# Kernel tuning notes

Measured on AMD Instinct MI355X. Metric: run time of the kernel, lower is better.

The kernel has to match this reference:

```python
import jax, jax.numpy as jnp
import numpy as np

N, E, G, H = 50000, 800000, 64, 4
IN_DIM, HID, OUT = 768, 256, 128
EPS = 1e-5
SLOPE = 0.2


def _glorot(k, shape):
    lim = np.sqrt(6.0 / (shape[0] + shape[1])).astype(np.float32)
    return jax.random.uniform(k, shape, jnp.float32, -lim, lim)


def setup_inputs() -> dict:
    key = jax.random.key(0)
    ks = jax.random.split(key, 24)
    inp = {
        'x': jax.random.normal(ks[0], (N, IN_DIM), jnp.float32),
        'edge_index': jax.random.randint(ks[1], (2, E), 0, N, jnp.int32),
        'batch': jnp.sort(jax.random.randint(ks[2], (N,), 0, G, jnp.int32)),
    }
    dims = [(IN_DIM, HID), (HID, HID), (HID, OUT)]
    for i, (di, do) in enumerate(dims, start=1):
        c = do // H
        inp[f'W{i}'] = _glorot(ks[3 * i], (di, do))
        inp[f'asrc{i}'] = _glorot(ks[3 * i + 1], (H, c))
        inp[f'adst{i}'] = _glorot(ks[3 * i + 2], (H, c))
        inp[f'b{i}'] = jnp.zeros((do,), jnp.float32)
        inp[f'g{i}'] = jnp.ones((do,), jnp.float32)
        inp[f'be{i}'] = jnp.zeros((do,), jnp.float32)
    return inp


def gat_conv(x, src, dst, W, asrc, adst, b):
    # PyG GATConv, concat=True, negative_slope=0.2, self-loops pre-appended.
    n = x.shape[0]
    HC = W.shape[1]
    C = HC // H
    h = (x @ W).reshape(n, H, C)                 # [N,H,C]
    e_src = (h * asrc).sum(-1)                   # [N,H]
    e_dst = (h * adst).sum(-1)                   # [N,H]
    e = jax.nn.leaky_relu(e_src[src] + e_dst[dst], SLOPE)  # [E',H]
    m = jax.ops.segment_max(e, dst, num_segments=n)
    p = jnp.exp(e - m[dst])
    denom = jax.ops.segment_sum(p, dst, num_segments=n)
    alpha = p / denom[dst]                       # segment softmax over in-edges
    out = jax.ops.segment_sum(alpha[:, :, None] * h[src], dst, num_segments=n)
    return out.reshape(n, HC) + b


def layer_norm(x, g, b):
    mu = x.mean(-1, keepdims=True)
    var = x.var(-1, keepdims=True)
    return g * (x - mu) * jax.lax.rsqrt(var + EPS) + b


def reference(x, edge_index, batch, W1, asrc1, adst1, b1, g1, be1,
              W2, asrc2, adst2, b2, g2, be2, W3, asrc3, adst3, b3, g3, be3):
    n = x.shape[0]
    loops = jnp.arange(n, dtype=edge_index.dtype)
    src = jnp.concatenate([edge_index[0], loops])
    dst = jnp.concatenate([edge_index[1], loops])
    h = gat_conv(x, src, dst, W1, asrc1, adst1, b1)
    h = layer_norm(jax.nn.elu(h), g1, be1)
    h = gat_conv(h, src, dst, W2, asrc2, adst2, b2)
    h = layer_norm(jax.nn.elu(h), g2, be2)
    h = gat_conv(h, src, dst, W3, asrc3, adst3, b3)
    node_emb = layer_norm(h, g3, be3)
    s = jax.ops.segment_sum(node_emb, batch, num_segments=G)
    cnt = jax.ops.segment_sum(jnp.ones((n, 1), node_emb.dtype), batch, num_segments=G)
    graph_emb = s / jnp.maximum(cnt, 1.0)
    return (node_emb, graph_emb)
```

## Files before the change

### kernel.cpp

```cpp
#include <hip/hip_runtime.h>
#include <math.h>

__device__ __forceinline__ float lrelu(float v) { return v > 0.f ? v : 0.2f * v; }
__device__ __forceinline__ float bf2f(ushort u) {
    return __uint_as_float(((unsigned int)u) << 16);
}
__device__ __forceinline__ ushort f2bf(float f) {
    unsigned int x = __float_as_uint(f);
    return (ushort)((x + 0x7fffu + ((x >> 16) & 1u)) >> 16);
}
__device__ __forceinline__ float wave_allred_sum(float v) {
#pragma unroll
    for (int off = 1; off < 64; off <<= 1) v += __shfl_xor(v, off, 64);
    return v;
}

typedef short bf16x8 __attribute__((ext_vector_type(8)));
typedef float f32x4 __attribute__((ext_vector_type(4)));

typedef const __attribute__((address_space(1))) void* gas_ptr;
typedef __attribute__((address_space(3))) void* las_ptr;
__device__ __forceinline__ void gload_lds16(const void* g, void* l) {
    __builtin_amdgcn_global_load_lds((gas_ptr)g, (las_ptr)l, 16, 0, 0);
}

__global__ void hist_kernel(const int* __restrict__ dstrow, int* __restrict__ cnt,
                            int Etot, int E) {
    int i = blockIdx.x * blockDim.x + threadIdx.x;
    if (i >= Etot) return;
    int d = (i < E) ? dstrow[i] : (i - E);
    atomicAdd(&cnt[d], 1);
}

__global__ __launch_bounds__(256) void scan1_kernel(const int* __restrict__ cnt,
                                                    int* __restrict__ out,
                                                    int* __restrict__ btot, int n) {
    __shared__ int s[256];
    int i = blockIdx.x * 256 + threadIdx.x;
    int v = (i < n) ? cnt[i] : 0;
    s[threadIdx.x] = v;
    __syncthreads();
    for (int off = 1; off < 256; off <<= 1) {
        int t = (threadIdx.x >= off) ? s[threadIdx.x - off] : 0;
        __syncthreads();
        s[threadIdx.x] += t;
        __syncthreads();
    }
    if (i < n) out[i] = s[threadIdx.x];
    if (threadIdx.x == 255) btot[blockIdx.x] = s[255];
}
__global__ __launch_bounds__(1024) void scan2_kernel(int* __restrict__ btot, int nb) {
    __shared__ int s[1024];
    int tid = threadIdx.x;
    int v = (tid < nb) ? btot[tid] : 0;
    s[tid] = v;
    __syncthreads();
    for (int off = 1; off < 1024; off <<= 1) {
        int t = (tid >= off) ? s[tid - off] : 0;
        __syncthreads();
        s[tid] += t;
        __syncthreads();
    }
    if (tid < nb) btot[tid] = s[tid] - v;
}
__global__ void scan3_kernel(const int* __restrict__ scanned, const int* __restrict__ btot,
                             int* __restrict__ rowptr, int n) {
    int i = blockIdx.x * 256 + threadIdx.x;
    if (i < n) rowptr[i + 1] = scanned[i] + btot[i >> 8];
    if (i == 0) rowptr[0] = 0;
}

__global__ void fill_kernel(const int* __restrict__ srcrow, const int* __restrict__ dstrow,
                            const int* __restrict__ rowptr, int* __restrict__ pos,
                            int* __restrict__ srcs, int Etot, int E) {
    int i = blockIdx.x * blockDim.x + threadIdx.x;
    if (i >= Etot) return;
    int d = (i < E) ? dstrow[i] : (i - E);
    int s = (i < E) ? srcrow[i] : (i - E);
    int p = atomicAdd(&pos[d], 1);
    srcs[rowptr[d] + p] = s;
}

__global__ __launch_bounds__(256) void wconv_kernel(const float* __restrict__ W,
                                                    ushort* __restrict__ Wt, int K, int N) {
    __shared__ float t[32][33];
    int k0 = blockIdx.x * 32, n0 = blockIdx.y * 32;
    int tx = threadIdx.x & 31, ty = threadIdx.x >> 5;
#pragma unroll
    for (int i = 0; i < 32; i += 8)
        t[ty + i][tx] = W[(size_t)(k0 + ty + i) * N + n0 + tx];
    __syncthreads();
#pragma unroll
    for (int i = 0; i < 32; i += 8)
        Wt[(size_t)(n0 + ty + i) * K + k0 + tx] = f2bf(t[tx][ty + i]);
}

template <typename TA>
__global__ __launch_bounds__(256) void gemm_mfma2(const TA* __restrict__ A,
                                                  const ushort* __restrict__ Wt,
                                                  ushort* __restrict__ C,
                                                  int M, int K, int N) {
    constexpr bool F32A = (sizeof(TA) == 4);
    constexpr int ASZ = F32A ? 16384 : 8192;
    __shared__ __align__(16) unsigned char smem[2 * ASZ + 16384];

    int tid = threadIdx.x;
    int wv = tid >> 6, lane = tid & 63;
    int quad = lane >> 4, mrow = lane & 15;

    int nwg = gridDim.x * gridDim.y;
    int id = blockIdx.y * gridDim.x + blockIdx.x;
    int q8 = nwg >> 3, r8 = nwg & 7;
    int xcd = id & 7, loc = id >> 3;
    int wgid = (xcd < r8 ? xcd * (q8 + 1) : r8 * (q8 + 1) + (xcd - r8) * q8) + loc;
    int n0 = (wgid % gridDim.x) * 128;
    int m0 = (wgid / gridDim.x) * 128;

    f32x4 acc[2][8] = {};

    auto stageA = [&](int kt, int buf) {
        unsigned char* lb = smem + buf * ASZ;
        if constexpr (F32A) {
#pragma unroll
            for (int q = 0; q < 4; q++) {
                int row = q * 32 + (tid >> 3);
                int gch = (tid & 7) ^ (row & 7);
                int rc = min(m0 + row, M - 1);
                gload_lds16((const float*)A + (size_t)rc * K + kt + gch * 4,
                            lb + q * 4096 + tid * 16);
            }
        } else {
#pragma unroll
            for (int q = 0; q < 2; q++) {
                int row = q * 64 + (tid >> 2);
                int gch = (tid & 3) ^ ((row & 3) ^ ((row >> 2) & 1));
                int rc = min(m0 + row, M - 1);
                gload_lds16((const ushort*)A + (size_t)rc * K + kt + gch * 8,
                            lb + q * 4096 + tid * 16);
            }
        }
    };
    auto stageB = [&](int kt, int buf) {
        unsigned char* lb = smem + 2 * ASZ + buf * 8192;
#pragma unroll
        for (int q = 0; q < 2; q++) {
            int row = q * 64 + (tid >> 2);
            int gch = (tid & 3) ^ ((row & 3) ^ ((row >> 2) & 1));
            gload_lds16(Wt + (size_t)(n0 + row) * K + kt + gch * 8,
                        lb + q * 4096 + tid * 16);
        }
    };

    int nsteps = K >> 5;
    stageA(0, 0);
    stageB(0, 0);
    __syncthreads();

    for (int s = 0; s < nsteps; s++) {
        int kt = s << 5;
        if (s + 1 < nsteps) {
            stageA(kt + 32, (s + 1) & 1);
            stageB(kt + 32, (s + 1) & 1);
        }
        const unsigned char* la = smem + (s & 1) * ASZ;
        const unsigned char* lbB = smem + 2 * ASZ + (s & 1) * 8192;

        bf16x8 afrag[2], bfrag[8];
#pragma unroll
        for (int r = 0; r < 2; r++) {
            int row = wv * 32 + r * 16 + mrow;
            if constexpr (F32A) {
                int f = row & 7;
                float4 x0 = *(const float4*)(la + row * 128 + ((quad * 2 + 0) ^ f) * 16);
                float4 x1 = *(const float4*)(la + row * 128 + ((quad * 2 + 1) ^ f) * 16);
                union { bf16x8 v; ushort u[8]; } t;
                t.u[0] = f2bf(x0.x); t.u[1] = f2bf(x0.y);
                t.u[2] = f2bf(x0.z); t.u[3] = f2bf(x0.w);
                t.u[4] = f2bf(x1.x); t.u[5] = f2bf(x1.y);
                t.u[6] = f2bf(x1.z); t.u[7] = f2bf(x1.w);
                afrag[r] = t.v;
            } else {
                int f = (row & 3) ^ ((row >> 2) & 1);
                afrag[r] = *(const bf16x8*)(la + row * 64 + (quad ^ f) * 16);
            }
        }
#pragma unroll
        for (int c = 0; c < 8; c++) {
            int row = c * 16 + mrow;
            int f = (row & 3) ^ ((row >> 2) & 1);
            bfrag[c] = *(const bf16x8*)(lbB + row * 64 + (quad ^ f) * 16);
        }
#pragma unroll
        for (int r = 0; r < 2; r++)
#pragma unroll
            for (int c = 0; c < 8; c++)
                acc[r][c] = __builtin_amdgcn_mfma_f32_16x16x32_bf16(afrag[r], bfrag[c],
                                                                    acc[r][c], 0, 0, 0);
        __syncthreads();
    }

    int col = lane & 15;
#pragma unroll
    for (int r = 0; r < 2; r++) {
#pragma unroll
        for (int c = 0; c < 8; c++) {
#pragma unroll
            for (int reg = 0; reg < 4; reg++) {
                int gm = m0 + wv * 32 + r * 16 + quad * 4 + reg;
                int gn = n0 + c * 16 + col;
                if (gm < M) C[(size_t)gm * N + gn] = f2bf(acc[r][c][reg]);
            }
        }
    }
}

template <int VPL>
__global__ __launch_bounds__(256) void attn_wave(const ushort* __restrict__ H,
                                                 const float* __restrict__ asrc,
                                                 const float* __restrict__ adst,
                                                 float* __restrict__ es, float* __restrict__ ed,
                                                 int N) {
    constexpr int HC = VPL * 64;
    int lane = threadIdx.x & 63;
    int node = (blockIdx.x * blockDim.x + threadIdx.x) >> 6;
    if (node >= N) return;
    const ushort* hp = H + (size_t)node * HC + lane * VPL;
    float esum = 0.f, dsum = 0.f;
#pragma unroll
    for (int j = 0; j < VPL; j++) {
        float h = bf2f(hp[j]);
        int ch = lane * VPL + j;
        esum += h * asrc[ch];
        dsum += h * adst[ch];
    }
#pragma unroll
    for (int off = 1; off < 16; off <<= 1) {
        esum += __shfl_xor(esum, off, 64);
        dsum += __shfl_xor(dsum, off, 64);
    }
    if ((lane & 15) == 0) {
        int hh = lane >> 4;
        es[node * 4 + hh] = esum;
        ed[node * 4 + hh] = dsum;
    }
}

template <int VPL>
__global__ __launch_bounds__(256) void agg_gather(
    const ushort* __restrict__ H, const float* __restrict__ es, const float* __restrict__ ed,
    const int* __restrict__ rowptr, const int* __restrict__ srcs,
    const float* __restrict__ bias, const float* __restrict__ gamma,
    const float* __restrict__ beta, ushort* __restrict__ XoutB, float* __restrict__ XoutF,
    int N, int applyElu) {
    constexpr int HC = VPL * 64;
    int lane = threadIdx.x & 63;
    int node = (blockIdx.x * blockDim.x + threadIdx.x) >> 6;
    if (node >= N) return;
    int base = rowptr[node];
    int deg = rowptr[node + 1] - base;
    float4 ed4 = *(const float4*)&ed[node * 4];

    float4 sm = make_float4(0.f, 0.f, 0.f, 0.f);
    for (int i = lane; i < deg; i += 64) {
        int s = srcs[base + i];
        float4 e4 = *(const float4*)&es[(size_t)s * 4];
        sm.x += __expf(lrelu(e4.x + ed4.x));
        sm.y += __expf(lrelu(e4.y + ed4.y));
        sm.z += __expf(lrelu(e4.z + ed4.z));
        sm.w += __expf(lrelu(e4.w + ed4.w));
    }
    sm.x = wave_allred_sum(sm.x); sm.y = wave_allred_sum(sm.y);
    sm.z = wave_allred_sum(sm.z); sm.w = wave_allred_sum(sm.w);

    int hh = lane >> 4;
    float rd_h = 1.f / ((hh == 0) ? sm.x : (hh == 1) ? sm.y : (hh == 2) ? sm.z : sm.w);
    float edh = (hh == 0) ? ed4.x : (hh == 1) ? ed4.y : (hh == 2) ? ed4.z : ed4.w;

    float acc[VPL];
#pragma unroll
    for (int j = 0; j < VPL; j++) acc[j] = 0.f;
    const ushort* Hl = H + lane * VPL;

    int i = 0;
    for (; i + 2 <= deg; i += 2) {
        int s0 = srcs[base + i];
        int s1 = srcs[base + i + 1];
        float e0 = es[(size_t)s0 * 4 + hh];
        float e1 = es[(size_t)s1 * 4 + hh];
        const ushort* hp0 = Hl + (size_t)s0 * HC;
        const ushort* hp1 = Hl + (size_t)s1 * HC;
        float a0 = __expf(lrelu(e0 + edh)) * rd_h;
        float a1 = __expf(lrelu(e1 + edh)) * rd_h;
        if constexpr (VPL == 4) {
            ushort4 h0 = *(const ushort4*)hp0;
            ushort4 h1 = *(const ushort4*)hp1;
            acc[0] += a0 * bf2f(h0.x) + a1 * bf2f(h1.x);
            acc[1] += a0 * bf2f(h0.y) + a1 * bf2f(h1.y);
            acc[2] += a0 * bf2f(h0.z) + a1 * bf2f(h1.z);
            acc[3] += a0 * bf2f(h0.w) + a1 * bf2f(h1.w);
        } else {
            ushort2 h0 = *(const ushort2*)hp0;
            ushort2 h1 = *(const ushort2*)hp1;
            acc[0] += a0 * bf2f(h0.x) + a1 * bf2f(h1.x);
            acc[1] += a0 * bf2f(h0.y) + a1 * bf2f(h1.y);
        }
    }
    for (; i < deg; i++) {
        int s = srcs[base + i];
        float a = __expf(lrelu(es[(size_t)s * 4 + hh] + edh)) * rd_h;
        const ushort* hp = Hl + (size_t)s * HC;
        if constexpr (VPL == 4) {
            ushort4 hv = *(const ushort4*)hp;
            acc[0] += a * bf2f(hv.x); acc[1] += a * bf2f(hv.y);
            acc[2] += a * bf2f(hv.z); acc[3] += a * bf2f(hv.w);
        } else {
            ushort2 hv = *(const ushort2*)hp;
            acc[0] += a * bf2f(hv.x); acc[1] += a * bf2f(hv.y);
        }
    }

    float v[VPL];
    float s1 = 0.f, s2 = 0.f;
#pragma unroll
    for (int j = 0; j < VPL; j++) {
        int ch = lane * VPL + j;
        float t = acc[j] + bias[ch];
        if (applyElu) t = (t > 0.f) ? t : (__expf(t) - 1.f);
        v[j] = t;
        s1 += t;
        s2 += t * t;
    }
    s1 = wave_allred_sum(s1);
    s2 = wave_allred_sum(s2);
    float mu = s1 / (float)HC;
    float var = s2 / (float)HC - mu * mu;
    float rs = rsqrtf(var + 1e-5f);
#pragma unroll
    for (int j = 0; j < VPL; j++) {
        int ch = lane * VPL + j;
        float o = gamma[ch] * (v[j] - mu) * rs + beta[ch];
        if (XoutF) XoutF[(size_t)node * HC + ch] = o;
        else XoutB[(size_t)node * HC + ch] = f2bf(o);
    }
}

__global__ __launch_bounds__(128) void gsum_kernel(const float* __restrict__ node_emb,
                                                   const int* __restrict__ batch,
                                                   float* __restrict__ gsum,
                                                   int* __restrict__ gcnt, int N) {
    int start = blockIdx.x * 256;
    if (start >= N) return;
    int end = min(start + 256, N);
    int ch = threadIdx.x;
    float acc = 0.f;
    int runlen = 0;
    int curg = batch[start];
    for (int n = start; n < end; n++) {
        int g = batch[n];
        if (g != curg) {
            atomicAdd(&gsum[curg * 128 + ch], acc);
            if (ch == 0) atomicAdd(&gcnt[curg], runlen);
            acc = 0.f; runlen = 0; curg = g;
        }
        acc += node_emb[(size_t)n * 128 + ch];
        runlen++;
    }
    atomicAdd(&gsum[curg * 128 + ch], acc);
    if (ch == 0) atomicAdd(&gcnt[curg], runlen);
}

__global__ void gfinal_kernel(const float* __restrict__ gsum, const int* __restrict__ gcnt,
                              float* __restrict__ out, int Gn) {
    int i = blockIdx.x * blockDim.x + threadIdx.x;
    if (i >= Gn * 128) return;
    int g = i >> 7;
    out[i] = gsum[i] / fmaxf((float)gcnt[g], 1.f);
}

extern "C" void kernel_launch(void* const* d_in, const int* in_sizes, int n_in, void* d_out,
                              int out_size, void* d_ws, size_t ws_size, hipStream_t stream) {
    const float* x = (const float*)d_in[0];
    const int* ei = (const int*)d_in[1];
    const int* batch = (const int*)d_in[2];
    const float* W1 = (const float*)d_in[3];
    const float* as1 = (const float*)d_in[4];
    const float* ad1 = (const float*)d_in[5];
    const float* b1 = (const float*)d_in[6];
    const float* g1 = (const float*)d_in[7];
    const float* be1 = (const float*)d_in[8];
    const float* W2 = (const float*)d_in[9];
    const float* as2 = (const float*)d_in[10];
    const float* ad2 = (const float*)d_in[11];
    const float* b2 = (const float*)d_in[12];
    const float* g2 = (const float*)d_in[13];
    const float* be2 = (const float*)d_in[14];
    const float* W3 = (const float*)d_in[15];
    const float* as3 = (const float*)d_in[16];
    const float* ad3 = (const float*)d_in[17];
    const float* b3 = (const float*)d_in[18];
    const float* g3 = (const float*)d_in[19];
    const float* be3 = (const float*)d_in[20];

    int N = in_sizes[2];
    int E = in_sizes[1] / 2;
    int Etot = E + N;

    char* w = (char*)d_ws;
    size_t off = 0;
    auto alloc = [&](size_t bytes) -> void* {
        void* p = w + off;
        off += (bytes + 255) & ~(size_t)255;
        return p;
    };
    int* cnt = (int*)alloc((size_t)N * 4);
    int* pos = (int*)alloc((size_t)N * 4);
    float* gsum = (float*)alloc(64 * 128 * 4);
    int* gcnt = (int*)alloc(64 * 4);
    size_t zbytes = off;
    int* scantmp = (int*)alloc((size_t)N * 4);
    int* btot = (int*)alloc(1024 * 4);
    int* rowptr = (int*)alloc((size_t)(N + 1) * 4);
    int* srcs = (int*)alloc((size_t)Etot * 4);
    float* es = (float*)alloc((size_t)N * 16);
    float* ed = (float*)alloc((size_t)N * 16);
    ushort* Hb = (ushort*)alloc((size_t)N * 256 * 2);
    ushort* Xb = (ushort*)alloc((size_t)N * 256 * 2);
    ushort* wt1 = (ushort*)alloc((size_t)768 * 256 * 2);
    ushort* wt2 = (ushort*)alloc((size_t)256 * 256 * 2);
    ushort* wt3 = (ushort*)alloc((size_t)256 * 128 * 2);

    hipMemsetAsync(d_ws, 0, zbytes, stream);

    const int* srcrow = ei;
    const int* dstrow = ei + E;

    wconv_kernel<<<dim3(768 / 32, 256 / 32), 256, 0, stream>>>(W1, wt1, 768, 256);
    wconv_kernel<<<dim3(256 / 32, 256 / 32), 256, 0, stream>>>(W2, wt2, 256, 256);
    wconv_kernel<<<dim3(256 / 32, 128 / 32), 256, 0, stream>>>(W3, wt3, 256, 128);

    int eb = (Etot + 255) / 256;
    int nb = (N + 255) / 256;
    hist_kernel<<<eb, 256, 0, stream>>>(dstrow, cnt, Etot, E);
    scan1_kernel<<<nb, 256, 0, stream>>>(cnt, scantmp, btot, N);
    scan2_kernel<<<1, 1024, 0, stream>>>(btot, nb);
    scan3_kernel<<<nb, 256, 0, stream>>>(scantmp, btot, rowptr, N);
    fill_kernel<<<eb, 256, 0, stream>>>(srcrow, dstrow, rowptr, pos, srcs, Etot, E);

    int mT = (N + 127) / 128;
    int nodeWaveBlocks = (N + 3) / 4;

    float* out_node = (float*)d_out;
    float* out_graph = (float*)d_out + (size_t)N * 128;

    gemm_mfma2<float><<<dim3(2, mT), 256, 0, stream>>>(x, wt1, Hb, N, 768, 256);
    attn_wave<4><<<nodeWaveBlocks, 256, 0, stream>>>(Hb, as1, ad1, es, ed, N);
    agg_gather<4><<<nodeWaveBlocks, 256, 0, stream>>>(Hb, es, ed, rowptr, srcs, b1, g1, be1,
                                                      Xb, nullptr, N, 1);
    gemm_mfma2<ushort><<<dim3(2, mT), 256, 0, stream>>>(Xb, wt2, Hb, N, 256, 256);
    attn_wave<4><<<nodeWaveBlocks, 256, 0, stream>>>(Hb, as2, ad2, es, ed, N);
    agg_gather<4><<<nodeWaveBlocks, 256, 0, stream>>>(Hb, es, ed, rowptr, srcs, b2, g2, be2,
                                                      Xb, nullptr, N, 1);
    gemm_mfma2<ushort><<<dim3(1, mT), 256, 0, stream>>>(Xb, wt3, Hb, N, 256, 128);
    attn_wave<2><<<nodeWaveBlocks, 256, 0, stream>>>(Hb, as3, ad3, es, ed, N);
    agg_gather<2><<<nodeWaveBlocks, 256, 0, stream>>>(Hb, es, ed, rowptr, srcs, b3, g3, be3,
                                                      nullptr, out_node, N, 0);
    gsum_kernel<<<(N + 255) / 256, 128, 0, stream>>>(out_node, batch, gsum, gcnt, N);
    gfinal_kernel<<<(64 * 128 + 255) / 256, 256, 0, stream>>>(gsum, gcnt, out_graph, 64);
}
```

Measured before the change: 770.9 us.

## Load GEMM operands directly from global into registers, dropping LDS staging

Replaces the LDS double-buffered GEMM with a version where each wave loads its A and B MFMA fragments straight from global memory into registers. A is prefetched two k-steps ahead in registers, and the block-wide __syncthreads per step is gone. The aim is to cut LDS traffic, barrier stalls and occupancy limits from shared memory. The cost is that B is no longer shared across the four waves through LDS, so each wave reloads the weight tile and leans on the caches, and the per-row global reads are less coalesced.

```diff
diff --git a/kernel.cpp b/kernel.cpp
--- a/kernel.cpp
+++ b/kernel.cpp
@@ -18,10 +18,11 @@
 typedef short bf16x8 __attribute__((ext_vector_type(8)));
 typedef float f32x4 __attribute__((ext_vector_type(4)));
 
-typedef const __attribute__((address_space(1))) void* gas_ptr;
-typedef __attribute__((address_space(3))) void* las_ptr;
-__device__ __forceinline__ void gload_lds16(const void* g, void* l) {
-    __builtin_amdgcn_global_load_lds((gas_ptr)g, (las_ptr)l, 16, 0, 0);
+__device__ __forceinline__ bf16x8 pack8(float4 lo, float4 hi) {
+    union { bf16x8 v; ushort u[8]; } t;
+    t.u[0] = f2bf(lo.x); t.u[1] = f2bf(lo.y); t.u[2] = f2bf(lo.z); t.u[3] = f2bf(lo.w);
+    t.u[4] = f2bf(hi.x); t.u[5] = f2bf(hi.y); t.u[6] = f2bf(hi.z); t.u[7] = f2bf(hi.w);
+    return t.v;
 }
 
 __global__ void hist_kernel(const int* __restrict__ dstrow, int* __restrict__ cnt,
@@ -96,14 +97,11 @@
 }
 
 template <typename TA>
-__global__ __launch_bounds__(256) void gemm_mfma2(const TA* __restrict__ A,
-                                                  const ushort* __restrict__ Wt,
-                                                  ushort* __restrict__ C,
-                                                  int M, int K, int N) {
+__global__ __launch_bounds__(256) void gemm_direct(const TA* __restrict__ A,
+                                                   const ushort* __restrict__ Wt,
+                                                   ushort* __restrict__ C,
+                                                   int M, int K, int N) {
     constexpr bool F32A = (sizeof(TA) == 4);
-    constexpr int ASZ = F32A ? 16384 : 8192;
-    __shared__ __align__(16) unsigned char smem[2 * ASZ + 16384];
-
     int tid = threadIdx.x;
     int wv = tid >> 6, lane = tid & 63;
     int quad = lane >> 4, mrow = lane & 15;
@@ -118,85 +116,73 @@
 
     f32x4 acc[2][8] = {};
 
-    auto stageA = [&](int kt, int buf) {
-        unsigned char* lb = smem + buf * ASZ;
-        if constexpr (F32A) {
-#pragma unroll
-            for (int q = 0; q < 4; q++) {
-                int row = q * 32 + (tid >> 3);
-                int gch = (tid & 7) ^ (row & 7);
-                int rc = min(m0 + row, M - 1);
-                gload_lds16((const float*)A + (size_t)rc * K + kt + gch * 4,
-                            lb + q * 4096 + tid * 16);
+    int g0 = min(m0 + wv * 32 + mrow, M - 1);
+    int g1 = min(m0 + wv * 32 + 16 + mrow, M - 1);
+    const TA* ap0 = A + (size_t)g0 * K + quad * 8;
+    const TA* ap1 = A + (size_t)g1 * K + quad * 8;
+    const ushort* bp = Wt + (size_t)(n0 + mrow) * K + quad * 8;
+
+    int nsteps = K >> 5;
+    int kmax = K - 32;
+
+    if constexpr (F32A) {
+        struct AF { float4 a, b, c, d; };
+        auto loadA = [&](int kt) {
+            AF r;
+            r.a = *(const float4*)(ap0 + kt);
+            r.b = *(const float4*)(ap0 + kt + 4);
+            r.c = *(const float4*)(ap1 + kt);
+            r.d = *(const float4*)(ap1 + kt + 4);
+            return r;
+        };
+        AF aC = loadA(0);
+        AF aN = loadA(min(32, kmax));
+        for (int s = 0; s < nsteps; s++) {
+            int kt = s << 5;
+            bf16x8 bfrag[8];
+#pragma unroll
+            for (int c = 0; c < 8; c++)
+                bfrag[c] = *(const bf16x8*)(bp + (size_t)(c * 16) * K + kt);
+            AF aNN = loadA(min(kt + 64, kmax));
+            bf16x8 af0 = pack8(aC.a, aC.b);
+            bf16x8 af1 = pack8(aC.c, aC.d);
+#pragma unroll
+            for (int c = 0; c < 8; c++) {
+                acc[0][c] = __builtin_amdgcn_mfma_f32_16x16x32_bf16(af0, bfrag[c],
+                                                                    acc[0][c], 0, 0, 0);
+                acc[1][c] = __builtin_amdgcn_mfma_f32_16x16x32_bf16(af1, bfrag[c],
+                                                                    acc[1][c], 0, 0, 0);
             }
-        } else {
-#pragma unroll
-            for (int q = 0; q < 2; q++) {
-                int row = q * 64 + (tid >> 2);
-                int gch = (tid & 3) ^ ((row & 3) ^ ((row >> 2) & 1));
-                int rc = min(m0 + row, M - 1);
-                gload_lds16((const ushort*)A + (size_t)rc * K + kt + gch * 8,
-                            lb + q * 4096 + tid * 16);
+            aC = aN;
+            aN = aNN;
+        }
+    } else {
+        struct AB { bf16x8 a, b; };
+        auto loadA = [&](int kt) {
+            AB r;
+            r.a = *(const bf16x8*)(ap0 + kt);
+            r.b = *(const bf16x8*)(ap1 + kt);
+            return r;
+        };
+        AB aC = loadA(0);
+        AB aN = loadA(min(32, kmax));
+        for (int s = 0; s < nsteps; s++) {
+            int kt = s << 5;
+            bf16x8 bfrag[8];
+#pragma unroll
+            for (int c = 0; c < 8; c++)
+                bfrag[c] = *(const bf16x8*)(bp + (size_t)(c * 16) * K + kt);
+            AB aNN = loadA(min(kt + 64, kmax));
+#pragma unroll
+            for (int c = 0; c < 8; c++) {
+                acc[0][c] = __builtin_amdgcn_mfma_f32_16x16x32_bf16(aC.a, bfrag[c],
+                                                                    acc[0][c], 0, 0, 0);
+                acc[1][c] = __builtin_amdgcn_mfma_f32_16x16x32_bf16(aC.b, bfrag[c],
+                                                                    acc[1][c], 0, 0, 0);
             }
-        }
-    };
-    auto stageB = [&](int kt, int buf) {
-        unsigned char* lb = smem + 2 * ASZ + buf * 8192;
-#pragma unroll
-        for (int q = 0; q < 2; q++) {
-            int row = q * 64 + (tid >> 2);
-            int gch = (tid & 3) ^ ((row & 3) ^ ((row >> 2) & 1));
-            gload_lds16(Wt + (size_t)(n0 + row) * K + kt + gch * 8,
-                        lb + q * 4096 + tid * 16);
-        }
-    };
-
-    int nsteps = K >> 5;
-    stageA(0, 0);
-    stageB(0, 0);
-    __syncthreads();
-
-    for (int s = 0; s < nsteps; s++) {
-        int kt = s << 5;
-        if (s + 1 < nsteps) {
-            stageA(kt + 32, (s + 1) & 1);
-            stageB(kt + 32, (s + 1) & 1);
-        }
-        const unsigned char* la = smem + (s & 1) * ASZ;
-        const unsigned char* lbB = smem + 2 * ASZ + (s & 1) * 8192;
-
-        bf16x8 afrag[2], bfrag[8];
-#pragma unroll
-        for (int r = 0; r < 2; r++) {
-            int row = wv * 32 + r * 16 + mrow;
-            if constexpr (F32A) {
-                int f = row & 7;
-                float4 x0 = *(const float4*)(la + row * 128 + ((quad * 2 + 0) ^ f) * 16);
-                float4 x1 = *(const float4*)(la + row * 128 + ((quad * 2 + 1) ^ f) * 16);
-                union { bf16x8 v; ushort u[8]; } t;
-                t.u[0] = f2bf(x0.x); t.u[1] = f2bf(x0.y);
-                t.u[2] = f2bf(x0.z); t.u[3] = f2bf(x0.w);
-                t.u[4] = f2bf(x1.x); t.u[5] = f2bf(x1.y);
-                t.u[6] = f2bf(x1.z); t.u[7] = f2bf(x1.w);
-                afrag[r] = t.v;
-            } else {
-                int f = (row & 3) ^ ((row >> 2) & 1);
-                afrag[r] = *(const bf16x8*)(la + row * 64 + (quad ^ f) * 16);
-            }
-        }
-#pragma unroll
-        for (int c = 0; c < 8; c++) {
-            int row = c * 16 + mrow;
-            int f = (row & 3) ^ ((row >> 2) & 1);
-            bfrag[c] = *(const bf16x8*)(lbB + row * 64 + (quad ^ f) * 16);
-        }
-#pragma unroll
-        for (int r = 0; r < 2; r++)
-#pragma unroll
-            for (int c = 0; c < 8; c++)
-                acc[r][c] = __builtin_amdgcn_mfma_f32_16x16x32_bf16(afrag[r], bfrag[c],
-                                                                    acc[r][c], 0, 0, 0);
-        __syncthreads();
+            aC = aN;
+            aN = aNN;
+        }
     }
 
     int col = lane & 15;
@@ -452,15 +438,15 @@
     float* out_node = (float*)d_out;
     float* out_graph = (float*)d_out + (size_t)N * 128;
 
-    gemm_mfma2<float><<<dim3(2, mT), 256, 0, stream>>>(x, wt1, Hb, N, 768, 256);
+    gemm_direct<float><<<dim3(2, mT), 256, 0, stream>>>(x, wt1, Hb, N, 768, 256);
     attn_wave<4><<<nodeWaveBlocks, 256, 0, stream>>>(Hb, as1, ad1, es, ed, N);
     agg_gather<4><<<nodeWaveBlocks, 256, 0, stream>>>(Hb, es, ed, rowptr, srcs, b1, g1, be1,
                                                       Xb, nullptr, N, 1);
-    gemm_mfma2<ushort><<<dim3(2, mT), 256, 0, stream>>>(Xb, wt2, Hb, N, 256, 256);
+    gemm_direct<ushort><<<dim3(2, mT), 256, 0, stream>>>(Xb, wt2, Hb, N, 256, 256);
     attn_wave<4><<<nodeWaveBlocks, 256, 0, stream>>>(Hb, as2, ad2, es, ed, N);
     agg_gather<4><<<nodeWaveBlocks, 256, 0, stream>>>(Hb, es, ed, rowptr, srcs, b2, g2, be2,
                                                       Xb, nullptr, N, 1);
-    gemm_mfma2<ushort><<<dim3(1, mT), 256, 0, stream>>>(Xb, wt3, Hb, N, 256, 128);
+    gemm_direct<ushort><<<dim3(1, mT), 256, 0, stream>>>(Xb, wt3, Hb, N, 256, 128);
     attn_wave<2><<<nodeWaveBlocks, 256, 0, stream>>>(Hb, as3, ad3, es, ed, N);
     agg_gather<2><<<nodeWaveBlocks, 256, 0, stream>>>(Hb, es, ed, rowptr, srcs, b3, g3, be3,
                                                       nullptr, out_node, N, 0);
```

After: 856.9 us. 1.11x slower.
